# Kernel tuning notes

Hardware: AMD Instinct MI355X
Metric: run time of the kernel (lower is better)

The kernel has to match this reference:

```python
import jax, jax.numpy as jnp
import numpy as np

N = 100000
E = 1600000
D_IN = 128
HEADS = 8
HEAD_DIM = 16  # hidden_channels // heads = 128 // 8
D_HID = HEADS * HEAD_DIM  # 128
D_OUT = 128
NEG_SLOPE = 0.2


def setup_inputs() -> dict:
    key = jax.random.key(0)
    ks = jax.random.split(key, 10)
    x = jax.random.normal(ks[0], (N, D_IN), dtype=jnp.float32)
    edge_index = jax.random.randint(ks[1], (2, E), 0, N, dtype=jnp.int64)
    s = 1.0 / np.sqrt(D_IN)
    W_gat = jax.random.uniform(ks[2], (D_IN, D_HID), minval=-s, maxval=s, dtype=jnp.float32)
    att_src = jax.random.uniform(ks[3], (HEADS, HEAD_DIM), minval=-s, maxval=s, dtype=jnp.float32)
    att_dst = jax.random.uniform(ks[4], (HEADS, HEAD_DIM), minval=-s, maxval=s, dtype=jnp.float32)
    b_gat = jnp.zeros((D_HID,), dtype=jnp.float32)
    so = 1.0 / np.sqrt(D_OUT)
    W_fc1 = jax.random.uniform(ks[5], (D_OUT, D_OUT), minval=-so, maxval=so, dtype=jnp.float32)
    b_fc1 = jax.random.uniform(ks[6], (D_OUT,), minval=-so, maxval=so, dtype=jnp.float32)
    W_fc2 = jax.random.uniform(ks[7], (D_OUT, D_OUT), minval=-so, maxval=so, dtype=jnp.float32)
    b_fc2 = jax.random.uniform(ks[8], (D_OUT,), minval=-so, maxval=so, dtype=jnp.float32)
    return {"x": x, "edge_index": edge_index, "W_gat": W_gat, "att_src": att_src,
            "att_dst": att_dst, "b_gat": b_gat, "W_fc1": W_fc1, "b_fc1": b_fc1,
            "W_fc2": W_fc2, "b_fc2": b_fc2}


def _gat_conv(x, src, dst, W_gat, att_src, att_dst, b_gat):
    n = x.shape[0]
    xp = (x @ W_gat).reshape(n, HEADS, HEAD_DIM)        # [N,H,C]
    a_src = jnp.einsum('nhc,hc->nh', xp, att_src)       # [N,H]
    a_dst = jnp.einsum('nhc,hc->nh', xp, att_dst)       # [N,H]
    e = jax.nn.leaky_relu(a_src[src] + a_dst[dst], NEG_SLOPE)  # [E,H]
    # segment softmax over edges grouped by destination node
    e_max = jax.ops.segment_max(e, dst, num_segments=n)
    e = jnp.exp(e - e_max[dst])
    e_sum = jax.ops.segment_sum(e, dst, num_segments=n)
    alpha = e / (e_sum[dst] + 1e-16)                    # [E,H]
    msg = xp[src] * alpha[:, :, None]                   # [E,H,C]
    out = jax.ops.segment_sum(msg, dst, num_segments=n) # [N,H,C]
    return out.reshape(n, D_HID) + b_gat


def reference(x, edge_index, W_gat, att_src, att_dst, b_gat, W_fc1, b_fc1, W_fc2, b_fc2):
    n = x.shape[0]
    # PyG GATConv default add_self_loops=True
    loops = jnp.arange(n, dtype=edge_index.dtype)
    src = jnp.concatenate([edge_index[0], loops])
    dst = jnp.concatenate([edge_index[1], loops])
    z = _gat_conv(x, src, dst, W_gat, att_src, att_dst, b_gat)
    z1 = z @ W_fc1 + b_fc1
    z2 = z @ W_fc2 + b_fc2
    return (z, z1, z2)
```

## Files before the change

### kernel.cpp

```cpp
#include <hip/hip_runtime.h>
#include <hip/hip_bf16.h>


#define NBUCK  256
#define BSHIFT 9
#define BNODES 512
#define IPB    8192

typedef __attribute__((ext_vector_type(8))) short bf16x8;
typedef __attribute__((ext_vector_type(4))) float f32x4;

static __device__ __forceinline__ short f2bf(float f) {
    __hip_bfloat16 h = __float2bfloat16(f);
    return *reinterpret_cast<short*>(&h);
}

__global__ __launch_bounds__(256) void k0_swizzle(
    const float* __restrict__ W0, const float* __restrict__ W1,
    const float* __restrict__ W2, const float* __restrict__ att_s,
    const float* __restrict__ att_d, unsigned short* __restrict__ S0,
    unsigned short* __restrict__ S1, unsigned short* __restrict__ S2,
    unsigned short* __restrict__ Sa, int* __restrict__ col_total)
{
    const int t = blockIdx.x * 256 + threadIdx.x;
    if (t < NBUCK) col_total[t] = 0;
    if (t < 3 * 2048) {
        const int m = t >> 11;
        const int r = t & 2047;
        const int tile = r >> 6;
        const int l    = r & 63;
        const int ks   = tile & 3;
        const int cb   = tile >> 2;
        const int c    = cb * 16 + (l & 15);
        const int kb   = ks * 32 + (l >> 4) * 8;
        const float* W = (m == 0) ? W0 : (m == 1) ? W1 : W2;
        unsigned short* S = (m == 0) ? S0 : (m == 1) ? S1 : S2;
        unsigned short* dst = S + ((size_t)tile * 64 + l) * 8;
#pragma unroll
        for (int j = 0; j < 8; ++j)
            dst[j] = (unsigned short)f2bf(W[(kb + j) * 128 + c]);
    } else if (t < 3 * 2048 + 256) {
        const int r  = t - 3 * 2048;
        const int ks = r >> 6;
        const int l  = r & 63;
        const int hp = l & 15;
        const int h  = hp & 7;
        const float* av = (hp < 8) ? (att_s + h * 16) : (att_d + h * 16);
        unsigned short* dst = Sa + ((size_t)ks * 64 + l) * 8;
#pragma unroll
        for (int j = 0; j < 8; ++j) {
            const int k = ks * 32 + (l >> 4) * 8 + j;
            float acc = 0.f;
#pragma unroll
            for (int u = 0; u < 16; ++u)
                acc += W0[k * 128 + h * 16 + u] * av[u];
            dst[j] = (unsigned short)f2bf(acc);
        }
    }
}

__global__ __launch_bounds__(256) void g1p1(
    const float* __restrict__ x, const unsigned short* __restrict__ Wswz,
    const unsigned short* __restrict__ Sa, unsigned short* __restrict__ xpb,
    float* __restrict__ a_src, float* __restrict__ a_dst,
    const int* __restrict__ ei, int* __restrict__ M, int* __restrict__ col_total,
    int n, int E, int g1b, int nblk)
{
    if ((int)blockIdx.x < g1b) {
        const int wid  = __builtin_amdgcn_readfirstlane(threadIdx.x >> 6);
        const int lane = threadIdx.x & 63;
        const int lr   = lane & 15;
        const int kg   = lane >> 4;
        const int rowbase = blockIdx.x * 128 + wid * 32;

        bf16x8 afr[2][4];
#pragma unroll
        for (int rt = 0; rt < 2; ++rt) {
            int row = rowbase + rt * 16 + lr;
            row = (row < n) ? row : (n - 1);
            const float* rp = x + (size_t)row * 128 + kg * 8;
#pragma unroll
            for (int ks = 0; ks < 4; ++ks) {
                const float4 v0 = *reinterpret_cast<const float4*>(rp + ks * 32);
                const float4 v1 = *reinterpret_cast<const float4*>(rp + ks * 32 + 4);
                bf16x8 a;
                a[0] = f2bf(v0.x); a[1] = f2bf(v0.y); a[2] = f2bf(v0.z); a[3] = f2bf(v0.w);
                a[4] = f2bf(v1.x); a[5] = f2bf(v1.y); a[6] = f2bf(v1.z); a[7] = f2bf(v1.w);
                afr[rt][ks] = a;
            }
        }

        f32x4 acc[2][8] = {};
#pragma unroll
        for (int cb = 0; cb < 8; ++cb) {
            const unsigned short* bp = Wswz + ((size_t)(cb * 4) * 64 + lane) * 8;
            bf16x8 bfr[4];
#pragma unroll
            for (int ks = 0; ks < 4; ++ks)
                bfr[ks] = *reinterpret_cast<const bf16x8*>(bp + (size_t)ks * 512);
#pragma unroll
            for (int ks = 0; ks < 4; ++ks) {
                acc[0][cb] = __builtin_amdgcn_mfma_f32_16x16x32_bf16(afr[0][ks], bfr[ks], acc[0][cb], 0, 0, 0);
                acc[1][cb] = __builtin_amdgcn_mfma_f32_16x16x32_bf16(afr[1][ks], bfr[ks], acc[1][cb], 0, 0, 0);
            }
        }

        f32x4 accs[2] = {};
#pragma unroll
        for (int ks = 0; ks < 4; ++ks) {
            const bf16x8 bs = *reinterpret_cast<const bf16x8*>(Sa + ((size_t)ks * 64 + lane) * 8);
            accs[0] = __builtin_amdgcn_mfma_f32_16x16x32_bf16(afr[0][ks], bs, accs[0], 0, 0, 0);
            accs[1] = __builtin_amdgcn_mfma_f32_16x16x32_bf16(afr[1][ks], bs, accs[1], 0, 0, 0);
        }

#pragma unroll
        for (int rt = 0; rt < 2; ++rt) {
#pragma unroll
            for (int reg = 0; reg < 4; ++reg) {
                const int row = rowbase + rt * 16 + kg * 4 + reg;
                if (row < n) {
                    unsigned short* op = xpb + (size_t)row * 128 + lr;
#pragma unroll
                    for (int cb = 0; cb < 8; ++cb)
                        op[cb * 16] = (unsigned short)f2bf(acc[rt][cb][reg]);
                    if (lr < 8) a_src[row * 8 + lr] = accs[rt][reg];
                    else        a_dst[row * 8 + (lr - 8)] = accs[rt][reg];
                }
            }
        }
    } else {
        __shared__ int h[NBUCK];
        const int pb  = blockIdx.x - g1b;
        const int tid = threadIdx.x;
        for (int k = tid; k < NBUCK; k += 256) h[k] = 0;
        __syncthreads();

        const int tot = E + n;
        const int base = pb * IPB;
        const int lim = (base + IPB < tot) ? base + IPB : tot;
        for (int j = base + tid; j < lim; j += 256) {
            const int d = (j < E) ? ei[E + j] : (j - E);
            atomicAdd(&h[d >> BSHIFT], 1);
        }
        __syncthreads();
        for (int k = tid; k < NBUCK; k += 256) {
            M[(size_t)k * nblk + pb] = h[k];
            if (h[k]) atomicAdd(&col_total[k], h[k]);
        }
    }
}

__global__ __launch_bounds__(256) void p2a_colscan(
    int* __restrict__ M, const int* __restrict__ col_total,
    int* __restrict__ bucket_ptr, int* __restrict__ row_ptr, int nblk, int N)
{
    const int b    = blockIdx.x;
    const int tid  = threadIdx.x;
    const int lane = tid & 63;
    const int wid  = tid >> 6;
    __shared__ int wsum[4];
    __shared__ int sbase;

    const int v0 = col_total[tid];
    int ws0 = v0;
#pragma unroll
    for (int off = 1; off < 64; off <<= 1) {
        const int t = __shfl_up(ws0, off);
        if (lane >= off) ws0 += t;
    }
    if (lane == 63) wsum[wid] = ws0;
    __syncthreads();
    int woff0 = 0;
    for (int w2 = 0; w2 < wid; ++w2) woff0 += wsum[w2];
    const int excl0 = woff0 + ws0 - v0;
    if (tid == b) sbase = excl0;
    if (b == NBUCK - 1 && tid == NBUCK - 1) {
        bucket_ptr[NBUCK] = excl0 + v0;
        row_ptr[N] = excl0 + v0;
    }
    __syncthreads();
    const int base = sbase;
    if (tid == 0) bucket_ptr[b] = base;
    __syncthreads();

    int carry = base;
    for (int bb = 0; bb < nblk; bb += 256) {
        const int idx = bb + tid;
        const int v = (idx < nblk) ? M[(size_t)b * nblk + idx] : 0;
        int ws = v;
#pragma unroll
        for (int off = 1; off < 64; off <<= 1) {
            const int t = __shfl_up(ws, off);
            if (lane >= off) ws += t;
        }
        if (lane == 63) wsum[wid] = ws;
        __syncthreads();
        int woff = 0;
        for (int w2 = 0; w2 < wid; ++w2) woff += wsum[w2];
        const int alltot = wsum[0] + wsum[1] + wsum[2] + wsum[3];
        if (idx < nblk) M[(size_t)b * nblk + idx] = carry + woff + ws - v;
        carry += alltot;
        __syncthreads();
    }
}

__global__ __launch_bounds__(256) void p3_scatter(
    const int* __restrict__ ei, const int* __restrict__ M,
    int* __restrict__ pairs, int E, int N, int nblk)
{
    __shared__ int lcnt[NBUCK];
    const int tid = threadIdx.x;
    for (int k = tid; k < NBUCK; k += 256) lcnt[k] = 0;
    __syncthreads();

    const int tot = E + N;
    const int base = blockIdx.x * IPB;
    const int lim = (base + IPB < tot) ? base + IPB : tot;
    for (int j = base + tid; j < lim; j += 256) {
        int s, d;
        if (j < E) { s = ei[j]; d = ei[E + j]; }
        else       { s = j - E; d = s; }
        const int b = d >> BSHIFT;
        const int r = atomicAdd(&lcnt[b], 1);
        const int pos = M[(size_t)b * nblk + blockIdx.x] + r;
        pairs[pos] = s | ((d & (BNODES - 1)) << 17);
    }
}

__global__ __launch_bounds__(256) void p4_finalize(
    const int* __restrict__ pairs, const int* __restrict__ bucket_ptr,
    int* __restrict__ row_ptr, int* __restrict__ csr_src, int N)
{
    const int b     = blockIdx.x;
    const int node0 = b << BSHIFT;
    const int beg   = bucket_ptr[b];
    const int end   = bucket_ptr[b + 1];
    const int tid   = threadIdx.x;
    const int lane  = tid & 63;
    const int wid   = tid >> 6;

    __shared__ int hist[BNODES];
    __shared__ int exc[BNODES];
    __shared__ int cnt2[BNODES];
    __shared__ int wsum[4];

    for (int k = tid; k < BNODES; k += 256) { hist[k] = 0; cnt2[k] = 0; }
    __syncthreads();

    for (int i = beg + tid; i < end; i += 256)
        atomicAdd(&hist[pairs[i] >> 17], 1);
    __syncthreads();

    const int a0 = hist[2 * tid];
    const int a1 = hist[2 * tid + 1];
    const int s  = a0 + a1;
    int ws = s;
#pragma unroll
    for (int off = 1; off < 64; off <<= 1) {
        const int t = __shfl_up(ws, off);
        if (lane >= off) ws += t;
    }
    if (lane == 63) wsum[wid] = ws;
    __syncthreads();
    int woff = 0;
    for (int w2 = 0; w2 < wid; ++w2) woff += wsum[w2];
    const int e0 = woff + ws - s;
    exc[2 * tid]     = e0;
    exc[2 * tid + 1] = e0 + a0;
    __syncthreads();

    for (int k = tid; k < BNODES; k += 256) {
        const int node = node0 + k;
        if (node < N) row_ptr[node] = beg + exc[k];
    }
    for (int i = beg + tid; i < end; i += 256) {
        const int v  = pairs[i];
        const int dl = v >> 17;
        const int r  = atomicAdd(&cnt2[dl], 1);
        csr_src[beg + exc[dl] + r] = v & 0x1FFFF;
    }
}

__global__ __launch_bounds__(256) void k5_aggregate(
    const unsigned short* __restrict__ xpb, const float* __restrict__ a_src,
    const float* __restrict__ a_dst, const int* __restrict__ row_ptr,
    const int* __restrict__ csr_src, const float* __restrict__ b_gat,
    float* __restrict__ z, unsigned int* __restrict__ zb, int n)
{
    const int wave = blockIdx.x * 4 + __builtin_amdgcn_readfirstlane(threadIdx.x >> 6);
    if (wave >= n) return;
    const int lane = threadIdx.x & 63;
    const int d = wave;
    const int beg = row_ptr[d];
    const int end = row_ptr[d + 1];
    const int h  = lane >> 3;
    const int jm = lane >> 3;
    const int hm = lane & 7;
    const float adst_hm = a_dst[d * 8 + hm];
    const int co = 2 * lane;

    float l0 = 0.f, l1 = 0.f;
    float ax0 = 0.f, ay0 = 0.f, ax1 = 0.f, ay1 = 0.f;

    for (int i = beg; i < end; i += 8) {
        const int idxm = (i + jm < end) ? (i + jm) : (end - 1);
        const int sm = csr_src[idxm];
        float v = a_src[(size_t)sm * 8 + hm] + adst_hm;
        v = (v > 0.f) ? v : 0.2f * v;
        float e = __expf(v);
        if (i + jm >= end) e = 0.f;

        int ss[8];
#pragma unroll
        for (int j = 0; j < 8; ++j) {
            const int idx = (i + j < end) ? (i + j) : (end - 1);
            ss[j] = csr_src[idx];
        }
        unsigned int xv[8];
#pragma unroll
        for (int j = 0; j < 8; ++j)
            xv[j] = *reinterpret_cast<const unsigned int*>(xpb + (size_t)ss[j] * 128 + co);
#pragma unroll
        for (int j = 0; j < 8; ++j) {
            const float pj = __shfl(e, (j << 3) + h);
            const float cx = __uint_as_float(xv[j] << 16);
            const float cy = __uint_as_float(xv[j] & 0xffff0000u);
            if (j & 1) {
                l1 += pj;
                ax1 = fmaf(pj, cx, ax1);
                ay1 = fmaf(pj, cy, ay1);
            } else {
                l0 += pj;
                ax0 = fmaf(pj, cx, ax0);
                ay0 = fmaf(pj, cy, ay0);
            }
        }
    }

    const float inv = 1.0f / (l0 + l1 + 1e-16f);
    const float2 bg = *reinterpret_cast<const float2*>(&b_gat[co]);
    float2 o;
    o.x = (ax0 + ax1) * inv + bg.x;
    o.y = (ay0 + ay1) * inv + bg.y;
    *reinterpret_cast<float2*>(&z[(size_t)d * 128 + co]) = o;
    const unsigned int pk = ((unsigned int)(unsigned short)f2bf(o.y) << 16) |
                            (unsigned int)(unsigned short)f2bf(o.x);
    zb[(size_t)d * 64 + lane] = pk;
}

__global__ __launch_bounds__(256) void g2_mfma_fc(
    const unsigned int* __restrict__ zb,
    const unsigned short* __restrict__ S1, const unsigned short* __restrict__ S2,
    const float* __restrict__ b1, const float* __restrict__ b2,
    float* __restrict__ z1, float* __restrict__ z2, int n)
{
    const int wid  = __builtin_amdgcn_readfirstlane(threadIdx.x >> 6);
    const int lane = threadIdx.x & 63;
    const int lr   = lane & 15;
    const int kg   = lane >> 4;
    const int rowbase = blockIdx.x * 128 + wid * 32;

    bf16x8 afr[2][4];
#pragma unroll
    for (int rt = 0; rt < 2; ++rt) {
        int row = rowbase + rt * 16 + lr;
        row = (row < n) ? row : (n - 1);
        const unsigned short* rp = (const unsigned short*)(zb + (size_t)row * 64) + kg * 8;
#pragma unroll
        for (int ks = 0; ks < 4; ++ks)
            afr[rt][ks] = *reinterpret_cast<const bf16x8*>(rp + ks * 32);
    }

    f32x4 acc1[2][8] = {};
    f32x4 acc2[2][8] = {};
#pragma unroll
    for (int cb = 0; cb < 8; ++cb) {
        const unsigned short* bp1 = S1 + ((size_t)(cb * 4) * 64 + lane) * 8;
        const unsigned short* bp2 = S2 + ((size_t)(cb * 4) * 64 + lane) * 8;
        bf16x8 f1[4], f2v[4];
#pragma unroll
        for (int ks = 0; ks < 4; ++ks) {
            f1[ks]  = *reinterpret_cast<const bf16x8*>(bp1 + (size_t)ks * 512);
            f2v[ks] = *reinterpret_cast<const bf16x8*>(bp2 + (size_t)ks * 512);
        }
#pragma unroll
        for (int ks = 0; ks < 4; ++ks) {
            acc1[0][cb] = __builtin_amdgcn_mfma_f32_16x16x32_bf16(afr[0][ks], f1[ks],  acc1[0][cb], 0, 0, 0);
            acc1[1][cb] = __builtin_amdgcn_mfma_f32_16x16x32_bf16(afr[1][ks], f1[ks],  acc1[1][cb], 0, 0, 0);
            acc2[0][cb] = __builtin_amdgcn_mfma_f32_16x16x32_bf16(afr[0][ks], f2v[ks], acc2[0][cb], 0, 0, 0);
            acc2[1][cb] = __builtin_amdgcn_mfma_f32_16x16x32_bf16(afr[1][ks], f2v[ks], acc2[1][cb], 0, 0, 0);
        }
    }

    float bb1[8], bb2[8];
#pragma unroll
    for (int cb = 0; cb < 8; ++cb) { bb1[cb] = b1[cb * 16 + lr]; bb2[cb] = b2[cb * 16 + lr]; }

#pragma unroll
    for (int rt = 0; rt < 2; ++rt) {
#pragma unroll
        for (int reg = 0; reg < 4; ++reg) {
            const int row = rowbase + rt * 16 + kg * 4 + reg;
            if (row < n) {
                float* o1 = z1 + (size_t)row * 128 + lr;
                float* o2 = z2 + (size_t)row * 128 + lr;
#pragma unroll
                for (int cb = 0; cb < 8; ++cb) {
                    o1[cb * 16] = acc1[rt][cb][reg] + bb1[cb];
                    o2[cb * 16] = acc2[rt][cb][reg] + bb2[cb];
                }
            }
        }
    }
}

extern "C" void kernel_launch(void* const* d_in, const int* in_sizes, int n_in,
                              void* d_out, int out_size, void* d_ws, size_t ws_size,
                              hipStream_t stream)
{
    const float* x       = (const float*)d_in[0];
    const int*   ei      = (const int*)  d_in[1];
    const float* W_gat   = (const float*)d_in[2];
    const float* att_src = (const float*)d_in[3];
    const float* att_dst = (const float*)d_in[4];
    const float* b_gat   = (const float*)d_in[5];
    const float* W_fc1   = (const float*)d_in[6];
    const float* b_fc1   = (const float*)d_in[7];
    const float* W_fc2   = (const float*)d_in[8];
    const float* b_fc2   = (const float*)d_in[9];

    const int N = in_sizes[0] / 128;
    const int E = in_sizes[1] / 2;
    const int tot = E + N;
    const int nblk = (tot + IPB - 1) / IPB;
    const int nbuck_used = (N + BNODES - 1) >> BSHIFT;
    const int g1b = (N + 127) / 128;

    char* w = (char*)d_ws;
    unsigned short* xpb = (unsigned short*)w;  w += (size_t)N * 128 * 2;
    unsigned int* zb = (unsigned int*)w;       w += (size_t)N * 64 * 4;
    float* a_src  = (float*)w;  w += (size_t)N * 8 * 4;
    float* a_dst  = (float*)w;  w += (size_t)N * 8 * 4;
    int* row_ptr  = (int*)w;    w += (size_t)(N + 1) * 4;
    w = (char*)(((size_t)w + 15) & ~(size_t)15);
    unsigned short* S0 = (unsigned short*)w; w += 16384 * 2;
    unsigned short* S1 = (unsigned short*)w; w += 16384 * 2;
    unsigned short* S2 = (unsigned short*)w; w += 16384 * 2;
    unsigned short* Sa = (unsigned short*)w; w += 2048 * 2;
    int* M          = (int*)w;  w += (size_t)nblk * NBUCK * 4;
    int* col_total  = (int*)w;  w += NBUCK * 4;
    int* bucket_ptr = (int*)w;  w += (NBUCK + 1) * 4;
    w = (char*)(((size_t)w + 15) & ~(size_t)15);
    int* pairs    = (int*)w;    w += (size_t)tot * 4;
    int* csr_src  = (int*)w;    w += (size_t)tot * 4;

    float* z  = (float*)d_out;
    float* z1 = z  + (size_t)N * 128;
    float* z2 = z1 + (size_t)N * 128;

    k0_swizzle<<<(3 * 2048 + 256 + 255) / 256, 256, 0, stream>>>(
        W_gat, W_fc1, W_fc2, att_src, att_dst, S0, S1, S2, Sa, col_total);

    g1p1<<<g1b + nblk, 256, 0, stream>>>(x, S0, Sa, xpb, a_src, a_dst,
                                         ei, M, col_total, N, E, g1b, nblk);

    p2a_colscan<<<NBUCK, 256, 0, stream>>>(M, col_total, bucket_ptr, row_ptr, nblk, N);
    p3_scatter<<<nblk, 256, 0, stream>>>(ei, M, pairs, E, N, nblk);
    p4_finalize<<<nbuck_used, 256, 0, stream>>>(pairs, bucket_ptr, row_ptr, csr_src, N);

    k5_aggregate<<<(N + 3) / 4, 256, 0, stream>>>(xpb, a_src, a_dst, row_ptr, csr_src,
                                                  b_gat, z, zb, N);

    g2_mfma_fc<<<(N + 127) / 128, 256, 0, stream>>>(zb, S1, S2, b_fc1, b_fc2, z1, z2, N);
}
```

Measured before the change: 206.0 us.

## Permute xp column layout for vectorized GEMM stores and matching aggregation

The projected features xp are stored in a permuted column order so each MFMA lane writes one 16-byte packed store per row instead of eight strided 2-byte stores. The aggregation kernel is adapted to the new layout: each lane now covers two columns from different heads, so it does two shuffles and keeps separate softmax denominators per column. The FC weight swizzle is permuted to match the reordered zb columns. The cost is extra shuffles and scattered 4-byte z stores in the aggregation kernel in exchange for coalesced xp writes.

```diff
diff --git a/kernel.cpp b/kernel.cpp
--- a/kernel.cpp
+++ b/kernel.cpp
@@ -37,8 +37,17 @@
         unsigned short* S = (m == 0) ? S0 : (m == 1) ? S1 : S2;
         unsigned short* dst = S + ((size_t)tile * 64 + l) * 8;
 #pragma unroll
-        for (int j = 0; j < 8; ++j)
-            dst[j] = (unsigned short)f2bf(W[(kb + j) * 128 + c]);
+        for (int j = 0; j < 8; ++j) {
+            const int p = kb + j;
+            int krow;
+            if (m == 0) {
+                krow = p;
+            } else {
+                const int w2 = p >> 1, hi = p & 1;
+                krow = 32 * (w2 & 3) + (w2 >> 2) + 16 * hi;
+            }
+            dst[j] = (unsigned short)f2bf(W[krow * 128 + c]);
+        }
     } else if (t < 3 * 2048 + 256) {
         const int r  = t - 3 * 2048;
         const int ks = r >> 6;
@@ -119,10 +128,16 @@
             for (int reg = 0; reg < 4; ++reg) {
                 const int row = rowbase + rt * 16 + kg * 4 + reg;
                 if (row < n) {
-                    unsigned short* op = xpb + (size_t)row * 128 + lr;
-#pragma unroll
-                    for (int cb = 0; cb < 8; ++cb)
-                        op[cb * 16] = (unsigned short)f2bf(acc[rt][cb][reg]);
+                    int4 pk;
+                    pk.x = (int)(((unsigned)(unsigned short)f2bf(acc[rt][1][reg]) << 16) |
+                                  (unsigned)(unsigned short)f2bf(acc[rt][0][reg]));
+                    pk.y = (int)(((unsigned)(unsigned short)f2bf(acc[rt][3][reg]) << 16) |
+                                  (unsigned)(unsigned short)f2bf(acc[rt][2][reg]));
+                    pk.z = (int)(((unsigned)(unsigned short)f2bf(acc[rt][5][reg]) << 16) |
+                                  (unsigned)(unsigned short)f2bf(acc[rt][4][reg]));
+                    pk.w = (int)(((unsigned)(unsigned short)f2bf(acc[rt][7][reg]) << 16) |
+                                  (unsigned)(unsigned short)f2bf(acc[rt][6][reg]));
+                    *reinterpret_cast<int4*>(xpb + (size_t)row * 128 + lr * 8) = pk;
                     if (lr < 8) a_src[row * 8 + lr] = accs[rt][reg];
                     else        a_dst[row * 8 + (lr - 8)] = accs[rt][reg];
                 }
@@ -293,14 +308,16 @@
     const int d = wave;
     const int beg = row_ptr[d];
     const int end = row_ptr[d + 1];
-    const int h  = lane >> 3;
+    const int c0 = 32 * (lane & 3) + (lane >> 2);
+    const int c1 = c0 + 16;
+    const int h0 = 2 * (lane & 3);
+    const int h1 = h0 + 1;
     const int jm = lane >> 3;
     const int hm = lane & 7;
     const float adst_hm = a_dst[d * 8 + hm];
-    const int co = 2 * lane;
-
-    float l0 = 0.f, l1 = 0.f;
-    float ax0 = 0.f, ay0 = 0.f, ax1 = 0.f, ay1 = 0.f;
+
+    float ls0a = 0.f, ls0b = 0.f, ls1a = 0.f, ls1b = 0.f;
+    float axa = 0.f, axb = 0.f, aya = 0.f, ayb = 0.f;
 
     for (int i = beg; i < end; i += 8) {
         const int idxm = (i + jm < end) ? (i + jm) : (end - 1);
@@ -319,33 +336,34 @@
         unsigned int xv[8];
 #pragma unroll
         for (int j = 0; j < 8; ++j)
-            xv[j] = *reinterpret_cast<const unsigned int*>(xpb + (size_t)ss[j] * 128 + co);
+            xv[j] = reinterpret_cast<const unsigned int*>(xpb + (size_t)ss[j] * 128)[lane];
 #pragma unroll
         for (int j = 0; j < 8; ++j) {
-            const float pj = __shfl(e, (j << 3) + h);
+            const float p0 = __shfl(e, (j << 3) + h0);
+            const float p1 = __shfl(e, (j << 3) + h1);
             const float cx = __uint_as_float(xv[j] << 16);
             const float cy = __uint_as_float(xv[j] & 0xffff0000u);
             if (j & 1) {
-                l1 += pj;
-                ax1 = fmaf(pj, cx, ax1);
-                ay1 = fmaf(pj, cy, ay1);
+                ls0b += p0; ls1b += p1;
+                axb = fmaf(p0, cx, axb);
+                ayb = fmaf(p1, cy, ayb);
             } else {
-                l0 += pj;
-                ax0 = fmaf(pj, cx, ax0);
-                ay0 = fmaf(pj, cy, ay0);
-            }
-        }
-    }
-
-    const float inv = 1.0f / (l0 + l1 + 1e-16f);
-    const float2 bg = *reinterpret_cast<const float2*>(&b_gat[co]);
-    float2 o;
-    o.x = (ax0 + ax1) * inv + bg.x;
-    o.y = (ay0 + ay1) * inv + bg.y;
-    *reinterpret_cast<float2*>(&z[(size_t)d * 128 + co]) = o;
-    const unsigned int pk = ((unsigned int)(unsigned short)f2bf(o.y) << 16) |
-                            (unsigned int)(unsigned short)f2bf(o.x);
-    zb[(size_t)d * 64 + lane] = pk;
+                ls0a += p0; ls1a += p1;
+                axa = fmaf(p0, cx, axa);
+                aya = fmaf(p1, cy, aya);
+            }
+        }
+    }
+
+    const float inv0 = 1.0f / (ls0a + ls0b + 1e-16f);
+    const float inv1 = 1.0f / (ls1a + ls1b + 1e-16f);
+    const float ox = (axa + axb) * inv0 + b_gat[c0];
+    const float oy = (aya + ayb) * inv1 + b_gat[c1];
+    z[(size_t)d * 128 + c0] = ox;
+    z[(size_t)d * 128 + c1] = oy;
+    zb[(size_t)d * 64 + lane] =
+        ((unsigned int)(unsigned short)f2bf(oy) << 16) |
+        (unsigned int)(unsigned short)f2bf(ox);
 }
 
 __global__ __launch_bounds__(256) void g2_mfma_fc(
```

Measured after the change: 204.5 us, median of 2. Within noise of the previous version (-0.7%).
